# Performance work log

Hardware: AMD Instinct MI355X
Metric: run time of the kernel (lower is better)

The kernel has to match this reference:

```python
import jax, jax.numpy as jnp
import numpy as np

EPS_RMS = 1e-6  # mmfreelm RMSNorm default eps

def _rmsnorm(x, w):
    var = jnp.mean(x * x, axis=-1, keepdims=True)
    return x * jax.lax.rsqrt(var + EPS_RMS) * w

def _activation_quant(x):
    # per-token absmax int8 quant (BitNet b1.58 activation quant)
    scale = 127.0 / jnp.clip(jnp.max(jnp.abs(x), axis=-1, keepdims=True), 1e-5)
    return jnp.clip(jnp.round(x * scale), -128.0, 127.0) / scale

def _weight_quant(w):
    # ternary quant with global mean-abs scale
    scale = 1.0 / jnp.clip(jnp.mean(jnp.abs(w)), 1e-5)
    return jnp.clip(jnp.round(w * scale), -1.0, 1.0) / scale

def _nm_mask(w, n, m):
    # keep top-n by |w| in every group of m along the input (last) dim
    O, I = w.shape
    g = jnp.abs(w).reshape(-1, m)            # [G, m]
    _, idx = jax.lax.top_k(g, n)             # [G, n]
    rows = jnp.arange(g.shape[0])[:, None]
    mask = jnp.zeros_like(g).at[rows, idx].set(1.0)
    return mask.reshape(O, I)

def setup_inputs() -> dict:
    key = jax.random.key(0)
    k1, k2 = jax.random.split(key)
    B, S, IN, OUT = 4, 2048, 4096, 11008
    x = jax.random.normal(k1, (B, S, IN), dtype=jnp.float32)
    weight = jax.random.normal(k2, (OUT, IN), dtype=jnp.float32) * 0.02
    norm_weight = jnp.ones((IN,), dtype=jnp.float32)
    return {"x": x, "weight": weight, "norm_weight": norm_weight,
            "sparse_n": 2, "sparse_m": 4}

def reference(x, weight, norm_weight, sparse_n, sparse_m):
    x_norm = _rmsnorm(x, norm_weight)
    # STE quantization (forward value == quantized value)
    x_q = x_norm + jax.lax.stop_gradient(_activation_quant(x_norm) - x_norm)
    w_q = weight + jax.lax.stop_gradient(_weight_quant(weight) - weight)
    mask = jax.lax.stop_gradient(_nm_mask(w_q, sparse_n, sparse_m))
    w_sparse = w_q * mask                    # [OUT, IN]
    return jnp.einsum('bsi,oi->bso', x_q, w_sparse)
```

## Files before the change

kernel.cpp:

```cpp
#include <hip/hip_runtime.h>
#include <stdint.h>

#define IN_DIM 4096
#define OUT_DIM 11008
#define TOKENS 8192
#define WN (45088768L)
#define NKT128 32

typedef int int4v __attribute__((ext_vector_type(4)));
#define AS1 __attribute__((address_space(1)))
#define AS3 __attribute__((address_space(3)))

__device__ __forceinline__ float bf2f(uint32_t u16) {
  union { uint32_t i; float f; } v; v.i = u16 << 16; return v.f;
}
__device__ __forceinline__ bool probe_bf16(const void* nw) {
  return ((const uint16_t*)nw)[0] == 0x3F80u;
}

__global__ __launch_bounds__(256) void k_wabs(const void* __restrict__ wv,
                                              const void* __restrict__ nwv,
                                              double* __restrict__ partial) {
  const bool b16 = probe_bf16(nwv);
  const long tid = (long)blockIdx.x * 256 + threadIdx.x;
  const long stride = (long)gridDim.x * 256;
  double s = 0.0;
  if (b16) {
    const uint4* w = (const uint4*)wv;
    for (long i = tid; i < WN / 8; i += stride) {
      uint4 v = w[i];
      uint32_t a[4] = {v.x, v.y, v.z, v.w};
      float t = 0.f;
#pragma unroll
      for (int j = 0; j < 4; j++)
        t += fabsf(bf2f(a[j] & 0xffffu)) + fabsf(bf2f(a[j] >> 16));
      s += (double)t;
    }
  } else {
    const float4* w = (const float4*)wv;
    for (long i = tid; i < WN / 4; i += stride) {
      float4 v = w[i];
      s += (double)(fabsf(v.x) + fabsf(v.y) + fabsf(v.z) + fabsf(v.w));
    }
  }
#pragma unroll
  for (int off = 32; off > 0; off >>= 1) s += __shfl_down(s, off);
  __shared__ double sd[4];
  if ((threadIdx.x & 63) == 0) sd[threadIdx.x >> 6] = s;
  __syncthreads();
  if (threadIdx.x == 0) partial[blockIdx.x] = (sd[0] + sd[1]) + (sd[2] + sd[3]);
}

__global__ __launch_bounds__(256) void k_wscale(const double* __restrict__ partial,
                                                float* __restrict__ hdr) {
  double s = 0.0;
  for (int i = threadIdx.x; i < 2048; i += 256) s += partial[i];
#pragma unroll
  for (int off = 32; off > 0; off >>= 1) s += __shfl_down(s, off);
  __shared__ double sd[4];
  if ((threadIdx.x & 63) == 0) sd[threadIdx.x >> 6] = s;
  __syncthreads();
  if (threadIdx.x == 0) {
    double mean = ((sd[0] + sd[1]) + (sd[2] + sd[3])) / (double)WN;
    float meanc = (float)mean;
    if (meanc < 1e-5f) meanc = 1e-5f;
    float wscale = 1.0f / meanc;
    hdr[0] = wscale;
    hdr[1] = 1.0f / wscale;
  }
}

__global__ __launch_bounds__(256) void k_act(const void* __restrict__ xv,
                                             const void* __restrict__ nwv,
                                             int8_t* __restrict__ qx,
                                             float* __restrict__ invsx) {
  const bool b16 = probe_bf16(nwv);
  const int t = blockIdx.x;
  const int tx = threadIdx.x;
  float xw[16];
  float ss = 0.f, mx = 0.f;
  if (b16) {
    const uint16_t* xr = (const uint16_t*)xv + (long)t * IN_DIM;
    const uint16_t* nw = (const uint16_t*)nwv;
#pragma unroll
    for (int c = 0; c < 2; c++) {
      uint4 vx = ((const uint4*)xr)[tx * 2 + c];
      uint4 vn = ((const uint4*)nw)[tx * 2 + c];
      uint32_t ax[4] = {vx.x, vx.y, vx.z, vx.w};
      uint32_t an[4] = {vn.x, vn.y, vn.z, vn.w};
#pragma unroll
      for (int j = 0; j < 4; j++) {
        float x0 = bf2f(ax[j] & 0xffffu), x1 = bf2f(ax[j] >> 16);
        float n0 = bf2f(an[j] & 0xffffu), n1 = bf2f(an[j] >> 16);
        ss += x0 * x0 + x1 * x1;
        float p0 = x0 * n0, p1 = x1 * n1;
        xw[c * 8 + j * 2]     = p0;
        xw[c * 8 + j * 2 + 1] = p1;
        mx = fmaxf(mx, fmaxf(fabsf(p0), fabsf(p1)));
      }
    }
  } else {
    const float* xr = (const float*)xv + (long)t * IN_DIM;
    const float* nw = (const float*)nwv;
#pragma unroll
    for (int c = 0; c < 4; c++) {
      float4 vx = ((const float4*)xr)[tx * 4 + c];
      float4 vn = ((const float4*)nw)[tx * 4 + c];
      ss += vx.x * vx.x + vx.y * vx.y + vx.z * vx.z + vx.w * vx.w;
      float p0 = vx.x * vn.x, p1 = vx.y * vn.y, p2 = vx.z * vn.z, p3 = vx.w * vn.w;
      xw[c * 4 + 0] = p0; xw[c * 4 + 1] = p1; xw[c * 4 + 2] = p2; xw[c * 4 + 3] = p3;
      mx = fmaxf(mx, fmaxf(fmaxf(fabsf(p0), fabsf(p1)), fmaxf(fabsf(p2), fabsf(p3))));
    }
  }
#pragma unroll
  for (int off = 32; off > 0; off >>= 1) {
    ss += __shfl_down(ss, off);
    mx = fmaxf(mx, __shfl_down(mx, off));
  }
  __shared__ float s_ss[4], s_mx[4];
  __shared__ float bc[1];
  if ((tx & 63) == 0) { s_ss[tx >> 6] = ss; s_mx[tx >> 6] = mx; }
  __syncthreads();
  if (tx == 0) {
    float sst = (s_ss[0] + s_ss[1]) + (s_ss[2] + s_ss[3]);
    float mxt = fmaxf(fmaxf(s_mx[0], s_mx[1]), fmaxf(s_mx[2], s_mx[3]));
    float var = sst / (float)IN_DIM;
    float rms = 1.0f / sqrtf(var + 1e-6f);
    float amax = rms * mxt;
    if (amax < 1e-5f) amax = 1e-5f;
    float scale = 127.0f / amax;
    bc[0] = rms * scale;
    invsx[t] = 1.0f / scale;
  }
  __syncthreads();
  float rsc = bc[0];
  uint32_t pw[4];
#pragma unroll
  for (int d = 0; d < 4; d++) {
    uint32_t v = 0;
#pragma unroll
    for (int j = 0; j < 4; j++) {
      float q = rintf(xw[d * 4 + j] * rsc);
      q = fminf(fmaxf(q, -128.f), 127.f);
      int qi = (int)q;
      v |= ((uint32_t)(qi & 0xff)) << (8 * j);
    }
    pw[d] = v;
  }
  uint4 st; st.x = pw[0]; st.y = pw[1]; st.z = pw[2]; st.w = pw[3];
  ((uint4*)(qx + (long)t * IN_DIM))[tx] = st;
}

__global__ __launch_bounds__(256) void k_wq(const void* __restrict__ wv,
                                            const void* __restrict__ nwv,
                                            const float* __restrict__ hdr,
                                            int8_t* __restrict__ qw) {
  const bool b16 = probe_bf16(nwv);
  const long i = (long)blockIdx.x * 256 + threadIdx.x;
  const float wscale = hdr[0];
  float f[8];
  if (b16) {
    uint4 v = ((const uint4*)wv)[i];
    uint32_t a[4] = {v.x, v.y, v.z, v.w};
#pragma unroll
    for (int j = 0; j < 4; j++) {
      f[j * 2]     = bf2f(a[j] & 0xffffu);
      f[j * 2 + 1] = bf2f(a[j] >> 16);
    }
  } else {
    float4 v0 = ((const float4*)wv)[i * 2];
    float4 v1 = ((const float4*)wv)[i * 2 + 1];
    f[0] = v0.x; f[1] = v0.y; f[2] = v0.z; f[3] = v0.w;
    f[4] = v1.x; f[5] = v1.y; f[6] = v1.z; f[7] = v1.w;
  }
  int q[8];
#pragma unroll
  for (int j = 0; j < 8; j++) {
    float qf = rintf(f[j] * wscale);
    qf = fminf(fmaxf(qf, -1.f), 1.f);
    q[j] = (int)qf;
  }
#pragma unroll
  for (int g = 0; g < 2; g++) {
    int cnt = 0;
#pragma unroll
    for (int j = 0; j < 4; j++) {
      int idx = g * 4 + j;
      if (q[idx] != 0) { cnt++; if (cnt > 2) q[idx] = 0; }
    }
  }
  uint32_t lo = 0, hi = 0;
#pragma unroll
  for (int j = 0; j < 4; j++) lo |= ((uint32_t)(q[j] & 0xff)) << (8 * j);
#pragma unroll
  for (int j = 0; j < 4; j++) hi |= ((uint32_t)(q[4 + j] & 0xff)) << (8 * j);
  uint2 st; st.x = lo; st.y = hi;
  ((uint2*)qw)[i] = st;
}

__global__ __launch_bounds__(512, 2) void k_gemm(const int8_t* __restrict__ qx,
                                                 const int8_t* __restrict__ qw,
                                                 const float* __restrict__ invsx,
                                                 const float* __restrict__ hdr,
                                                 float* __restrict__ out) {
  __shared__ __align__(16) int8_t sA[2][256 * 128];
  __shared__ __align__(16) int8_t sB[2][256 * 128];

  const int tx = threadIdx.x;
  const int wave = tx >> 6, lane = tx & 63;
  const int wr = wave >> 2, wc = wave & 3;
  const int fr = lane & 15;
  const int fg = lane >> 4;

  const int bid = blockIdx.x;
  const int swz = (bid & 7) * 172 + (bid >> 3);
  const int m0 = (swz & 31) * 256;
  const int n0 = (swz >> 5) * 256;

  const int srow = tx >> 3;
  const int scol = ((tx & 7) ^ ((tx >> 4) & 7)) * 16;
  const int8_t* gA = qx + (long)(m0 + srow) * IN_DIM + scol;
  const int8_t* gB = qw + (long)(n0 + srow) * IN_DIM + scol;
  int8_t* const sA0 = &sA[0][0];
  int8_t* const sB0 = &sB[0][0];

  auto STAGE = [&](int t) {
    if (t >= NKT128) return;
    int8_t* bA = sA0 + (t & 1) * (256 * 128);
    int8_t* bB = sB0 + (t & 1) * (256 * 128);
    const long ko = (long)t * 128;
#pragma unroll
    for (int rb = 0; rb < 256; rb += 64) {
      __builtin_amdgcn_global_load_lds(
          (const AS1 void*)(gA + ko + (long)rb * IN_DIM),
          (AS3 void*)(bA + rb * 128 + wave * 1024), 16, 0, 0);
      __builtin_amdgcn_global_load_lds(
          (const AS1 void*)(gB + ko + (long)rb * IN_DIM),
          (AS3 void*)(bB + rb * 128 + wave * 1024), 16, 0, 0);
    }
  };

  int offA[8][2], offB[4][2];
#pragma unroll
  for (int mi = 0; mi < 8; ++mi) {
    const int row = wr * 128 + mi * 16 + fr;
    const int xr = (row >> 1) & 7;
#pragma unroll
    for (int ks = 0; ks < 2; ++ks)
      offA[mi][ks] = row * 128 + (((ks * 4 + fg) ^ xr) * 16);
  }
#pragma unroll
  for (int ni = 0; ni < 4; ++ni) {
    const int row = wc * 64 + ni * 16 + fr;
    const int xr = (row >> 1) & 7;
#pragma unroll
    for (int ks = 0; ks < 2; ++ks)
      offB[ni][ks] = row * 128 + (((ks * 4 + fg) ^ xr) * 16);
  }

  int4v acc[8][4];
#pragma unroll
  for (int mi = 0; mi < 8; ++mi)
#pragma unroll
    for (int ni = 0; ni < 4; ++ni) {
      acc[mi][ni][0] = 0; acc[mi][ni][1] = 0; acc[mi][ni][2] = 0; acc[mi][ni][3] = 0;
    }

  STAGE(0);
  __syncthreads();

  for (int t = 0; t < NKT128; ++t) {
    const int bofs = (t & 1) * (256 * 128);

    STAGE(t + 1);

    int4v a[8][2], b[4][2];
#pragma unroll
    for (int ni = 0; ni < 4; ++ni) {
      b[ni][0] = *(const int4v*)(sB0 + bofs + offB[ni][0]);
      b[ni][1] = *(const int4v*)(sB0 + bofs + offB[ni][1]);
    }
#pragma unroll
    for (int mi = 0; mi < 8; ++mi) {
      a[mi][0] = *(const int4v*)(sA0 + bofs + offA[mi][0]);
      a[mi][1] = *(const int4v*)(sA0 + bofs + offA[mi][1]);
    }

    __builtin_amdgcn_s_setprio(1);
#pragma unroll
    for (int mi = 0; mi < 8; ++mi)
#pragma unroll
      for (int ni = 0; ni < 4; ++ni)
#pragma unroll
        for (int ks = 0; ks < 2; ++ks)
          acc[mi][ni] = __builtin_amdgcn_mfma_i32_16x16x64_i8(a[mi][ks], b[ni][ks], acc[mi][ni], 0, 0, 0);
    __builtin_amdgcn_s_setprio(0);

    __syncthreads();
  }

  const float winv = hdr[1];
#pragma unroll
  for (int mi = 0; mi < 8; ++mi) {
    const int rbase = m0 + wr * 128 + mi * 16 + (lane >> 4) * 4;
#pragma unroll
    for (int r = 0; r < 4; ++r) {
      const int trow = rbase + r;
      const float fs = invsx[trow] * winv;
      const long ob = (long)trow * OUT_DIM + n0 + wc * 64 + fr;
#pragma unroll
      for (int ni = 0; ni < 4; ++ni) {
        out[ob + ni * 16] = (float)acc[mi][ni][r] * fs;
      }
    }
  }
}

extern "C" void kernel_launch(void* const* d_in, const int* in_sizes, int n_in,
                              void* d_out, int out_size, void* d_ws, size_t ws_size,
                              hipStream_t stream) {
  const void* x  = d_in[0];
  const void* w  = d_in[1];
  const void* nw = d_in[2];
  float* out = (float*)d_out;

  char* ws = (char*)d_ws;
  float*  hdr     = (float*)ws;
  double* partial = (double*)(ws + 1024);
  float*  invsx   = (float*)(ws + 20480);
  int8_t* qx      = (int8_t*)(ws + (1L << 20));
  int8_t* qw      = (int8_t*)(ws + 36L * (1L << 20));

  hipLaunchKernelGGL(k_wabs,   dim3(2048),   dim3(256), 0, stream, w, nw, partial);
  hipLaunchKernelGGL(k_wscale, dim3(1),      dim3(256), 0, stream, partial, hdr);
  hipLaunchKernelGGL(k_act,    dim3(TOKENS), dim3(256), 0, stream, x, nw, qx, invsx);
  hipLaunchKernelGGL(k_wq,     dim3(22016),  dim3(256), 0, stream, w, nw, hdr, qw);
  hipLaunchKernelGGL(k_gemm,   dim3(32 * 43), dim3(512), 0, stream,
                     qx, qw, invsx, hdr, out);
}
```

Before: 631.4 us.

## Load activation fragments directly from global memory, drop A shared-memory staging

```diff
diff --git a/kernel.cpp b/kernel.cpp
--- a/kernel.cpp
+++ b/kernel.cpp
@@ -203,7 +203,6 @@
                                                  const float* __restrict__ invsx,
                                                  const float* __restrict__ hdr,
                                                  float* __restrict__ out) {
-  __shared__ __align__(16) int8_t sA[2][256 * 128];
   __shared__ __align__(16) int8_t sB[2][256 * 128];
 
   const int tx = threadIdx.x;
@@ -214,41 +213,28 @@
 
   const int bid = blockIdx.x;
   const int swz = (bid & 7) * 172 + (bid >> 3);
-  const int m0 = (swz & 31) * 256;
-  const int n0 = (swz >> 5) * 256;
+  const int bm = swz / 43;
+  const int bn = swz % 43;
+  const int m0 = bm * 256, n0 = bn * 256;
 
   const int srow = tx >> 3;
   const int scol = ((tx & 7) ^ ((tx >> 4) & 7)) * 16;
-  const int8_t* gA = qx + (long)(m0 + srow) * IN_DIM + scol;
   const int8_t* gB = qw + (long)(n0 + srow) * IN_DIM + scol;
-  int8_t* const sA0 = &sA[0][0];
   int8_t* const sB0 = &sB[0][0];
 
   auto STAGE = [&](int t) {
     if (t >= NKT128) return;
-    int8_t* bA = sA0 + (t & 1) * (256 * 128);
     int8_t* bB = sB0 + (t & 1) * (256 * 128);
     const long ko = (long)t * 128;
 #pragma unroll
     for (int rb = 0; rb < 256; rb += 64) {
-      __builtin_amdgcn_global_load_lds(
-          (const AS1 void*)(gA + ko + (long)rb * IN_DIM),
-          (AS3 void*)(bA + rb * 128 + wave * 1024), 16, 0, 0);
       __builtin_amdgcn_global_load_lds(
           (const AS1 void*)(gB + ko + (long)rb * IN_DIM),
           (AS3 void*)(bB + rb * 128 + wave * 1024), 16, 0, 0);
     }
   };
 
-  int offA[8][2], offB[4][2];
-#pragma unroll
-  for (int mi = 0; mi < 8; ++mi) {
-    const int row = wr * 128 + mi * 16 + fr;
-    const int xr = (row >> 1) & 7;
-#pragma unroll
-    for (int ks = 0; ks < 2; ++ks)
-      offA[mi][ks] = row * 128 + (((ks * 4 + fg) ^ xr) * 16);
-  }
+  int offB[4][2];
 #pragma unroll
   for (int ni = 0; ni < 4; ++ni) {
     const int row = wc * 64 + ni * 16 + fr;
@@ -258,6 +244,8 @@
       offB[ni][ks] = row * 128 + (((ks * 4 + fg) ^ xr) * 16);
   }
 
+  const int8_t* gA = qx + (long)(m0 + wr * 128 + fr) * IN_DIM + fg * 16;
+
   int4v acc[8][4];
 #pragma unroll
   for (int mi = 0; mi < 8; ++mi)
@@ -274,16 +262,19 @@
 
     STAGE(t + 1);
 
-    int4v a[8][2], b[4][2];
+    int4v a[8][2];
+    const long ka = (long)t * 128;
+#pragma unroll
+    for (int mi = 0; mi < 8; ++mi)
+#pragma unroll
+      for (int ks = 0; ks < 2; ++ks)
+        a[mi][ks] = *(const int4v*)(gA + (long)mi * 16 * IN_DIM + ka + ks * 64);
+
+    int4v b[4][2];
 #pragma unroll
     for (int ni = 0; ni < 4; ++ni) {
       b[ni][0] = *(const int4v*)(sB0 + bofs + offB[ni][0]);
       b[ni][1] = *(const int4v*)(sB0 + bofs + offB[ni][1]);
-    }
-#pragma unroll
-    for (int mi = 0; mi < 8; ++mi) {
-      a[mi][0] = *(const int4v*)(sA0 + bofs + offA[mi][0]);
-      a[mi][1] = *(const int4v*)(sA0 + bofs + offA[mi][1]);
     }
 
     __builtin_amdgcn_s_setprio(1);
```

Measured after the change: 1.049 ms. 66.1% more time.

## Restructure int8 GEMM main loop into 4-stage 64-wide K pipeline with split phases

Applied to the files above, without the earlier changes.

```diff
diff --git a/kernel.cpp b/kernel.cpp
--- a/kernel.cpp
+++ b/kernel.cpp
@@ -5,7 +5,7 @@
 #define OUT_DIM 11008
 #define TOKENS 8192
 #define WN (45088768L)
-#define NKT128 32
+#define NKT64 64
 
 typedef int int4v __attribute__((ext_vector_type(4)));
 #define AS1 __attribute__((address_space(1)))
@@ -203,8 +203,8 @@
                                                  const float* __restrict__ invsx,
                                                  const float* __restrict__ hdr,
                                                  float* __restrict__ out) {
-  __shared__ __align__(16) int8_t sA[2][256 * 128];
-  __shared__ __align__(16) int8_t sB[2][256 * 128];
+  __shared__ __align__(16) int8_t sA[4][256 * 64];
+  __shared__ __align__(16) int8_t sB[4][256 * 64];
 
   const int tx = threadIdx.x;
   const int wave = tx >> 6, lane = tx & 63;
@@ -217,45 +217,42 @@
   const int m0 = (swz & 31) * 256;
   const int n0 = (swz >> 5) * 256;
 
-  const int srow = tx >> 3;
-  const int scol = ((tx & 7) ^ ((tx >> 4) & 7)) * 16;
+  const int srow = tx >> 2;
+  const int scol = ((tx & 3) ^ ((srow >> 1) & 3)) * 16;
   const int8_t* gA = qx + (long)(m0 + srow) * IN_DIM + scol;
   const int8_t* gB = qw + (long)(n0 + srow) * IN_DIM + scol;
   int8_t* const sA0 = &sA[0][0];
   int8_t* const sB0 = &sB[0][0];
 
-  auto STAGE = [&](int t) {
-    if (t >= NKT128) return;
-    int8_t* bA = sA0 + (t & 1) * (256 * 128);
-    int8_t* bB = sB0 + (t & 1) * (256 * 128);
-    const long ko = (long)t * 128;
-#pragma unroll
-    for (int rb = 0; rb < 256; rb += 64) {
-      __builtin_amdgcn_global_load_lds(
-          (const AS1 void*)(gA + ko + (long)rb * IN_DIM),
-          (AS3 void*)(bA + rb * 128 + wave * 1024), 16, 0, 0);
-      __builtin_amdgcn_global_load_lds(
-          (const AS1 void*)(gB + ko + (long)rb * IN_DIM),
-          (AS3 void*)(bB + rb * 128 + wave * 1024), 16, 0, 0);
-    }
+  auto stageA = [&](int t) {
+    if (t >= NKT64) return;
+    int8_t* bA = sA0 + (t & 3) * 16384;
+    const long ko = (long)t * 64;
+    __builtin_amdgcn_global_load_lds(
+        (const AS1 void*)(gA + ko), (AS3 void*)(bA + wave * 1024), 16, 0, 0);
+    __builtin_amdgcn_global_load_lds(
+        (const AS1 void*)(gA + ko + 128L * IN_DIM), (AS3 void*)(bA + 8192 + wave * 1024), 16, 0, 0);
   };
-
-  int offA[8][2], offB[4][2];
+  auto stageB = [&](int t) {
+    if (t >= NKT64) return;
+    int8_t* bB = sB0 + (t & 3) * 16384;
+    const long ko = (long)t * 64;
+    __builtin_amdgcn_global_load_lds(
+        (const AS1 void*)(gB + ko), (AS3 void*)(bB + wave * 1024), 16, 0, 0);
+    __builtin_amdgcn_global_load_lds(
+        (const AS1 void*)(gB + ko + 128L * IN_DIM), (AS3 void*)(bB + 8192 + wave * 1024), 16, 0, 0);
+  };
+
+  int offA[8], offB[4];
 #pragma unroll
   for (int mi = 0; mi < 8; ++mi) {
     const int row = wr * 128 + mi * 16 + fr;
-    const int xr = (row >> 1) & 7;
-#pragma unroll
-    for (int ks = 0; ks < 2; ++ks)
-      offA[mi][ks] = row * 128 + (((ks * 4 + fg) ^ xr) * 16);
+    offA[mi] = row * 64 + ((fg ^ ((row >> 1) & 3)) * 16);
   }
 #pragma unroll
   for (int ni = 0; ni < 4; ++ni) {
     const int row = wc * 64 + ni * 16 + fr;
-    const int xr = (row >> 1) & 7;
-#pragma unroll
-    for (int ks = 0; ks < 2; ++ks)
-      offB[ni][ks] = row * 128 + (((ks * 4 + fg) ^ xr) * 16);
+    offB[ni] = row * 64 + ((fg ^ ((row >> 1) & 3)) * 16);
   }
 
   int4v acc[8][4];
@@ -266,37 +263,52 @@
       acc[mi][ni][0] = 0; acc[mi][ni][1] = 0; acc[mi][ni][2] = 0; acc[mi][ni][3] = 0;
     }
 
-  STAGE(0);
-  __syncthreads();
-
-  for (int t = 0; t < NKT128; ++t) {
-    const int bofs = (t & 1) * (256 * 128);
-
-    STAGE(t + 1);
-
-    int4v a[8][2], b[4][2];
-#pragma unroll
-    for (int ni = 0; ni < 4; ++ni) {
-      b[ni][0] = *(const int4v*)(sB0 + bofs + offB[ni][0]);
-      b[ni][1] = *(const int4v*)(sB0 + bofs + offB[ni][1]);
-    }
-#pragma unroll
-    for (int mi = 0; mi < 8; ++mi) {
-      a[mi][0] = *(const int4v*)(sA0 + bofs + offA[mi][0]);
-      a[mi][1] = *(const int4v*)(sA0 + bofs + offA[mi][1]);
-    }
-
+  stageA(0); stageB(0); stageA(1); stageB(1); stageA(2); stageB(2);
+  asm volatile("s_waitcnt vmcnt(8)" ::: "memory");
+  __builtin_amdgcn_s_barrier();
+
+  for (int t = 0; t < NKT64; ++t) {
+    const int ofs = (t & 3) * 16384;
+
+    int4v a[8], b01[2];
+#pragma unroll
+    for (int j = 0; j < 2; ++j) b01[j] = *(const int4v*)(sB0 + ofs + offB[j]);
+#pragma unroll
+    for (int mi = 0; mi < 8; ++mi) a[mi] = *(const int4v*)(sA0 + ofs + offA[mi]);
+    stageA(t + 3);
+    asm volatile("s_waitcnt lgkmcnt(8)" ::: "memory");
+    __builtin_amdgcn_s_barrier();
+    asm volatile("s_waitcnt lgkmcnt(0)" ::: "memory");
     __builtin_amdgcn_s_setprio(1);
 #pragma unroll
     for (int mi = 0; mi < 8; ++mi)
 #pragma unroll
-      for (int ni = 0; ni < 4; ++ni)
-#pragma unroll
-        for (int ks = 0; ks < 2; ++ks)
-          acc[mi][ni] = __builtin_amdgcn_mfma_i32_16x16x64_i8(a[mi][ks], b[ni][ks], acc[mi][ni], 0, 0, 0);
+      for (int j = 0; j < 2; ++j)
+        acc[mi][j] = __builtin_amdgcn_mfma_i32_16x16x64_i8(a[mi], b01[j], acc[mi][j], 0, 0, 0);
     __builtin_amdgcn_s_setprio(0);
-
-    __syncthreads();
+    __builtin_amdgcn_s_barrier();
+
+    int4v b23[2];
+#pragma unroll
+    for (int j = 0; j < 2; ++j) b23[j] = *(const int4v*)(sB0 + ofs + offB[2 + j]);
+    stageB(t + 3);
+    __builtin_amdgcn_s_barrier();
+    asm volatile("s_waitcnt lgkmcnt(0)" ::: "memory");
+    __builtin_amdgcn_s_setprio(1);
+#pragma unroll
+    for (int mi = 0; mi < 8; ++mi)
+#pragma unroll
+      for (int j = 0; j < 2; ++j)
+        acc[mi][2 + j] = __builtin_amdgcn_mfma_i32_16x16x64_i8(a[mi], b23[j], acc[mi][2 + j], 0, 0, 0);
+    __builtin_amdgcn_s_setprio(0);
+    if (t < NKT64 - 3) {
+      asm volatile("s_waitcnt vmcnt(8)" ::: "memory");
+    } else if (t == NKT64 - 3) {
+      asm volatile("s_waitcnt vmcnt(4)" ::: "memory");
+    } else if (t == NKT64 - 2) {
+      asm volatile("s_waitcnt vmcnt(0)" ::: "memory");
+    }
+    __builtin_amdgcn_s_barrier();
   }
 
   const float winv = hdr[1];
```

Result: no change. 642.6 us (+1.8%).
